# Performance work log

Measured on AMD Instinct MI355X. Metric: run time of the kernel, lower is better.

Reference implementation:

```python
import jax, jax.numpy as jnp
import numpy as np

B, C, H, W = 8, 384, 32, 32
NUM_HEADS = 8
HEAD_DIM = C // NUM_HEADS


def setup_inputs() -> dict:
    key = jax.random.key(0)
    k1, k2, k3, k4, k5 = jax.random.split(key, 5)
    s = 1.0 / np.sqrt(C)
    return {
        "x": jax.random.normal(k1, (B, C, H, W), dtype=jnp.float32),
        "w_qkv": jax.random.normal(k2, (3 * C, C), dtype=jnp.float32) * s,   # 1x1 conv == linear over channels
        "b_qkv": jax.random.normal(k3, (3 * C,), dtype=jnp.float32) * 0.01,
        "w_proj": jax.random.normal(k4, (C, C), dtype=jnp.float32) * s,
        "b_proj": jax.random.normal(k5, (C,), dtype=jnp.float32) * 0.01,
    }


def reference(x, w_qkv, b_qkv, w_proj, b_proj):
    b, c, h, w = x.shape
    n = h * w
    scale = HEAD_DIM ** (-0.5)
    # 1x1 conv qkv: (B, 3C, H, W)
    qkv = jnp.einsum('bchw,oc->bohw', x, w_qkv) + b_qkv[None, :, None, None]
    # 'b (three hd d) h0 w0 -> three b hd (h0 w0) d'
    qkv = qkv.reshape(b, 3, NUM_HEADS, HEAD_DIM, n)
    qkv = jnp.transpose(qkv, (1, 0, 2, 4, 3))  # (3, B, heads, N, d)
    q, k, v = qkv[0], qkv[1], qkv[2]
    attn = jnp.einsum('bhnd,bhmd->bhnm', q, k) * scale
    attn = jax.nn.softmax(attn, axis=-1)
    out = jnp.einsum('bhnm,bhmd->bhnd', attn, v)          # (B, heads, N, d)
    out = jnp.transpose(out, (0, 1, 3, 2)).reshape(b, c, h, w)  # b (hd d) h w
    out = jnp.einsum('bchw,oc->bohw', out, w_proj) + b_proj[None, :, None, None]
    return out
```

## Files before the change

### kernel.cpp

```cpp
#include <hip/hip_runtime.h>
#include <hip/hip_bf16.h>

typedef __hip_bfloat16 bf16;
typedef __bf16 bfx8 __attribute__((ext_vector_type(8)));
typedef float f32x4 __attribute__((ext_vector_type(4)));

#define Bk   8
#define Ck   384
#define NHk  8
#define Dk   48
#define Dp   64
#define Nk   1024
#define O3   1152


__device__ __forceinline__ void gload_lds16(const bf16* src, void* dst)
{
    __builtin_amdgcn_global_load_lds(
        (const __attribute__((address_space(1))) void*)src,
        (__attribute__((address_space(3))) void*)dst, 16, 0, 0);
}

__device__ __forceinline__ int pack2(float a, float b)
{
    bf16 ha = __float2bfloat16(a), hb = __float2bfloat16(b);
    unsigned lo = *(unsigned short*)&ha, hi = *(unsigned short*)&hb;
    return (int)(lo | (hi << 16));
}

__device__ __forceinline__ ushort4 pack4(float v0, float v1, float v2, float v3)
{
    bf16 h0 = __float2bfloat16(v0), h1 = __float2bfloat16(v1);
    bf16 h2 = __float2bfloat16(v2), h3 = __float2bfloat16(v3);
    ushort4 pk;
    pk.x = *(unsigned short*)&h0; pk.y = *(unsigned short*)&h1;
    pk.z = *(unsigned short*)&h2; pk.w = *(unsigned short*)&h3;
    return pk;
}

__global__ __launch_bounds__(256) void prep_kernel(
    const float* __restrict__ x, bf16* __restrict__ Xs,
    const float* __restrict__ wq, const float* __restrict__ wp,
    bf16* __restrict__ Wq, bf16* __restrict__ Wp,
    bf16* __restrict__ Qs, bf16* __restrict__ Ks)
{
    const int u = blockIdx.x * 256 + threadIdx.x;
    if (u < 393216) {
        int n = u & 1023, rest = u >> 10;
        int oct = rest % 48, b = rest / 48;
        const float* xb = x + (size_t)b * Ck * Nk;
        float f[8];
        #pragma unroll
        for (int e = 0; e < 8; ++e) f[e] = xb[(size_t)(oct * 8 + e) * Nk + n];
        int4 v = { pack2(f[0], f[1]), pack2(f[2], f[3]),
                   pack2(f[4], f[5]), pack2(f[6], f[7]) };
        bf16* dst = Xs + ((size_t)b * 64 + (n >> 4)) * 6144 + oct * 128 + (n & 15) * 8;
        *(int4*)dst = v;
    } else if (u < 448512) {
        int u1 = u - 393216;
        int o = u1 % 1152, oct = u1 / 1152;
        const float* src = wq + (size_t)o * Ck + oct * 8;
        int4 v = { pack2(src[0], src[1]), pack2(src[2], src[3]),
                   pack2(src[4], src[5]), pack2(src[6], src[7]) };
        bf16* dst = Wq + ((size_t)(o >> 4) * 48 + oct) * 128 + (o & 15) * 8;
        *(int4*)dst = v;
    } else if (u < 466944) {
        int u2 = u - 448512;
        int o = u2 % 384, oct = u2 / 384;
        const float* src = wp + (size_t)o * Ck + oct * 8;
        int4 v = { pack2(src[0], src[1]), pack2(src[2], src[3]),
                   pack2(src[4], src[5]), pack2(src[6], src[7]) };
        bf16* dst = Wp + ((size_t)(o >> 4) * 48 + oct) * 128 + (o & 15) * 8;
        *(int4*)dst = v;
    } else {
        int i = u - 466944;
        int buf = i >> 17;
        int r17 = i & 131071;
        int head = r17 >> 11;
        int r11 = r17 & 2047;
        int g = r11 >> 5, c5 = r11 & 31;
        int cd = 6 + (c5 >> 4), e = c5 & 15;
        bf16* p = (buf ? Ks : Qs) + (size_t)head * 65536 +
                  ((size_t)g * 8 + cd) * 128 + e * 8;
        *(int4*)p = (int4){0, 0, 0, 0};
    }
}

__global__ __launch_bounds__(256) void qkv_mfma_kernel(
    const bf16* __restrict__ Xs, const bf16* __restrict__ Wq,
    const float* __restrict__ bias,
    bf16* __restrict__ Qs, bf16* __restrict__ Ks, bf16* __restrict__ Vs)
{
    __shared__ __align__(16) bf16 Wl[24576];

    const int b    = blockIdx.z;
    const int by   = blockIdx.y;
    const int bx   = blockIdx.x;
    const int o0   = by * 64;
    const int n0   = bx * 128;
    const int wave = threadIdx.x >> 6;
    const int lane = threadIdx.x & 63;
    const int l15  = lane & 15, quad = lane >> 4;
    const int t3   = o0 / Ck;

    {
        const bf16* wsrc = Wq + (size_t)by * 24576;
        #pragma unroll
        for (int i = 0; i < 12; ++i) {
            int f = wave * 12 + i;
            gload_lds16(wsrc + f * 512 + lane * 8, (char*)Wl + f * 1024);
        }
    }

    const bf16* xg[2];
    #pragma unroll
    for (int i = 0; i < 2; ++i)
        xg[i] = Xs + ((size_t)(b * 64 + bx * 8 + wave * 2 + i) * 48) * 128 + lane * 8;
    const bf16* wl = Wl + lane * 8;

    f32x4 acc[8];
    #pragma unroll
    for (int i = 0; i < 8; ++i) acc[i] = (f32x4){0.f, 0.f, 0.f, 0.f};

    asm volatile("s_waitcnt vmcnt(0)" ::: "memory");
    __syncthreads();

    if (t3 < 2) {
        #pragma unroll
        for (int s = 0; s < 12; ++s) {
            bfx8 fx[2], fw[4];
            #pragma unroll
            for (int i = 0; i < 2; ++i) fx[i] = *(const bfx8*)(xg[i] + s * 512);
            #pragma unroll
            for (int j = 0; j < 4; ++j) fw[j] = *(const bfx8*)(wl + j * 6144 + s * 512);
            #pragma unroll
            for (int j = 0; j < 4; ++j)
                #pragma unroll
                for (int i = 0; i < 2; ++i)
                    acc[j * 2 + i] = __builtin_amdgcn_mfma_f32_16x16x32_bf16(
                        fw[j], fx[i], acc[j * 2 + i], 0, 0, 0);
        }
        const float qscale = 0.2082350964f;
        #pragma unroll
        for (int j = 0; j < 4; ++j) {
            int ob = o0 + j * 16 + quad * 4;
            float4 bi = *(const float4*)&bias[ob];
            int r  = ob - t3 * Ck;
            int hd = r / Dk, d0 = r - hd * Dk;
            bf16* hb = (t3 == 0 ? Qs : Ks) + (size_t)(b * NHk + hd) * 65536
                     + (d0 >> 3) * 128 + (d0 & 7);
            #pragma unroll
            for (int i = 0; i < 2; ++i) {
                int npos = n0 + wave * 32 + i * 16 + l15;
                f32x4 a = acc[j * 2 + i];
                float v0 = a[0] + bi.x, v1 = a[1] + bi.y;
                float v2 = a[2] + bi.z, v3 = a[3] + bi.w;
                if (t3 == 0) { v0 *= qscale; v1 *= qscale; v2 *= qscale; v3 *= qscale; }
                *(ushort4*)(hb + (size_t)(npos >> 4) * 1024 + (npos & 15) * 8) =
                    pack4(v0, v1, v2, v3);
            }
        }
    } else {
        #pragma unroll
        for (int s = 0; s < 12; ++s) {
            bfx8 fx[2], fw[4];
            #pragma unroll
            for (int i = 0; i < 2; ++i) fx[i] = *(const bfx8*)(xg[i] + s * 512);
            #pragma unroll
            for (int j = 0; j < 4; ++j) fw[j] = *(const bfx8*)(wl + j * 6144 + s * 512);
            #pragma unroll
            for (int i = 0; i < 2; ++i)
                #pragma unroll
                for (int j = 0; j < 4; ++j)
                    acc[i * 4 + j] = __builtin_amdgcn_mfma_f32_16x16x32_bf16(
                        fx[i], fw[j], acc[i * 4 + j], 0, 0, 0);
        }
        #pragma unroll
        for (int j = 0; j < 4; ++j) {
            int ov = o0 + j * 16 + l15;
            float bi = bias[ov];
            int r  = ov - 2 * Ck;
            int hd = r / Dk, d = r - hd * Dk;
            bf16* vbp = Vs + (size_t)(b * NHk + hd) * 49152
                      + (size_t)(d >> 4) * 16384 + (d & 15) * 8;
            #pragma unroll
            for (int i = 0; i < 2; ++i) {
                int npb = n0 + wave * 32 + i * 16 + quad * 4;
                f32x4 a = acc[i * 4 + j];
                *(ushort4*)(vbp + (size_t)(npb >> 3) * 128 + (npb & 7)) =
                    pack4(a[0] + bi, a[1] + bi, a[2] + bi, a[3] + bi);
            }
        }
    }
}

__global__ __launch_bounds__(256, 2) void attn_kernel(
    const bf16* __restrict__ Qs, const bf16* __restrict__ Ks,
    const bf16* __restrict__ Vs, bf16* __restrict__ AO)
{
    __shared__ __align__(16) bf16 KbL[2][4096];
    __shared__ __align__(16) bf16 VbL[2][3072];
    __shared__ __align__(16) short Ps[4 * 2 * 1152];
    __shared__ float sums[4][2][16];

    const int hd   = blockIdx.x;
    const int b    = blockIdx.y;
    const int bx   = blockIdx.z;
    const int t    = threadIdx.x;
    const int wave = t >> 6;
    const int lane = t & 63;
    const int l15  = lane & 15;
    const int quad = lane >> 4;
    const int grp16 = (bx * 4 + wave) * 2;

    const bf16* qb = Qs + (size_t)(b * NHk + hd) * 65536;
    const bf16* kb = Ks + (size_t)(b * NHk + hd) * 65536;
    const bf16* vb = Vs + (size_t)(b * NHk + hd) * 49152;

    auto stage = [&](int buf, int k0) {
        const bf16* ksrc = kb + (size_t)k0 * 64;
        const bf16* vsrc = vb + (size_t)(k0 >> 3) * 128;
        char* kdst = (char*)&KbL[buf][0];
        char* vdst = (char*)&VbL[buf][0];
        #pragma unroll
        for (int i = 0; i < 4; ++i) {
            const int l = wave + i * 4;
            if (l < 14) {
                const int piece = l >> 1, half = l & 1;
                const bf16* src; char* dst;
                if (piece < 4) {
                    src = ksrc + piece * 1024 + half * 512 + lane * 8;
                    dst = kdst + piece * 2048 + half * 1024;
                } else {
                    const int dc = piece - 4;
                    src = vsrc + (size_t)dc * 16384 + half * 512 + lane * 8;
                    dst = vdst + dc * 2048 + half * 1024;
                }
                gload_lds16(src, dst);
            }
        }
    };

    stage(0, 0);

    bfx8 bq[2][2];
    #pragma unroll
    for (int qt = 0; qt < 2; ++qt) {
        const bf16* qp = qb + ((size_t)(grp16 + qt) * 8 + quad) * 128 + l15 * 8;
        bq[qt][0] = *(const bfx8*)(qp);
        bq[qt][1] = *(const bfx8*)(qp + 512);
    }

    float l_run[2] = {0.f, 0.f};
    f32x4 oacc[2][3];
    #pragma unroll
    for (int qt = 0; qt < 2; ++qt)
        #pragma unroll
        for (int dc = 0; dc < 3; ++dc) oacc[qt][dc] = (f32x4){0.f, 0.f, 0.f, 0.f};

    short* const PsW[2] = { Ps + wave * 2304, Ps + wave * 2304 + 1152 };
    const int lo = quad * 128 + l15 * 8;

    asm volatile("s_waitcnt vmcnt(0)" ::: "memory");
    __syncthreads();

    auto step = [&](int buf, int k0, bool pf) {
        if (pf) stage(buf ^ 1, k0 + 64);

        const bf16* Kc = &KbL[buf][0];
        const bf16* Vc = &VbL[buf][0];

        f32x4 sf[2][4];
        #pragma unroll
        for (int s = 0; s < 4; ++s) {
            const bfx8 kf0 = *(const bfx8*)(Kc + s * 1024 + lo);
            const bfx8 kf1 = *(const bfx8*)(Kc + s * 1024 + 512 + lo);
            #pragma unroll
            for (int qt = 0; qt < 2; ++qt) {
                f32x4 z = (f32x4){0.f, 0.f, 0.f, 0.f};
                z = __builtin_amdgcn_mfma_f32_16x16x32_bf16(kf0, bq[qt][0], z, 0, 0, 0);
                z = __builtin_amdgcn_mfma_f32_16x16x32_bf16(kf1, bq[qt][1], z, 0, 0, 0);
                sf[qt][s] = z;
            }
        }

        #pragma unroll
        for (int qt = 0; qt < 2; ++qt) {
            float lsum = 0.f;
            #pragma unroll
            for (int s = 0; s < 4; ++s) {
                float e0 = __builtin_amdgcn_exp2f(sf[qt][s][0]);
                float e1 = __builtin_amdgcn_exp2f(sf[qt][s][1]);
                float e2 = __builtin_amdgcn_exp2f(sf[qt][s][2]);
                float e3 = __builtin_amdgcn_exp2f(sf[qt][s][3]);
                lsum += (e0 + e1) + (e2 + e3);
                *(ushort4*)&PsW[qt][l15 * 72 + s * 16 + quad * 4] =
                    pack4(e0, e1, e2, e3);
            }
            l_run[qt] += lsum;
        }

        #pragma unroll
        for (int qt = 0; qt < 2; ++qt) {
            const bfx8 ap0 = *(const bfx8*)&PsW[qt][l15 * 72 + quad * 8];
            const bfx8 ap1 = *(const bfx8*)&PsW[qt][l15 * 72 + 32 + quad * 8];
            #pragma unroll
            for (int dc = 0; dc < 3; ++dc) {
                const bfx8 bv0 = *(const bfx8*)(Vc + dc * 1024 + lo);
                const bfx8 bv1 = *(const bfx8*)(Vc + dc * 1024 + 512 + lo);
                oacc[qt][dc] = __builtin_amdgcn_mfma_f32_16x16x32_bf16(
                    ap0, bv0, oacc[qt][dc], 0, 0, 0);
                oacc[qt][dc] = __builtin_amdgcn_mfma_f32_16x16x32_bf16(
                    ap1, bv1, oacc[qt][dc], 0, 0, 0);
            }
        }

        asm volatile("s_waitcnt vmcnt(0)" ::: "memory");
        __syncthreads();
    };

    #pragma unroll 1
    for (int k0 = 0; k0 < Nk; k0 += 128) {
        step(0, k0, true);
        step(1, k0 + 64, k0 + 128 < Nk);
    }

    #pragma unroll
    for (int qt = 0; qt < 2; ++qt) {
        float lt = l_run[qt];
        lt += __shfl_xor(lt, 16, 64);
        lt += __shfl_xor(lt, 32, 64);
        sums[wave][qt][l15] = lt;
    }
    asm volatile("s_waitcnt lgkmcnt(0)" ::: "memory");

    #pragma unroll
    for (int qt = 0; qt < 2; ++qt) {
        short* OsW = PsW[qt];
        #pragma unroll
        for (int r = 0; r < 4; ++r) {
            int qi = quad * 4 + r;
            float rli = 1.0f / sums[wave][qt][qi];
            #pragma unroll
            for (int dcc = 0; dcc < 3; ++dcc) {
                bf16 hb = __float2bfloat16(oacc[qt][dcc][r] * rli);
                OsW[qi * 64 + dcc * 16 + l15] = *(short*)&hb;
            }
        }
    }
    asm volatile("s_waitcnt lgkmcnt(0)" ::: "memory");

    #pragma unroll
    for (int qt = 0; qt < 2; ++qt) {
        bf16* aob = AO + (((size_t)b * 64 + grp16 + qt) * 48 + hd * 6) * 128;
        short* OsW = PsW[qt];
        int u = lane;
        int4 v = *(const int4*)&OsW[(u & 15) * 64 + (u >> 4) * 8];
        *(int4*)(aob + u * 8) = v;
        if (lane < 32) {
            int u2 = 64 + lane;
            int4 v2 = *(const int4*)&OsW[(u2 & 15) * 64 + (u2 >> 4) * 8];
            *(int4*)(aob + u2 * 8) = v2;
        }
    }
}

__global__ __launch_bounds__(256) void proj_mfma_kernel(
    const bf16* __restrict__ AO, const bf16* __restrict__ Wp,
    const float* __restrict__ bias, float* __restrict__ out)
{
    __shared__ __align__(16) bf16 Wl[24576];

    const int b    = blockIdx.z;
    const int by   = blockIdx.y;
    const int bx   = blockIdx.x;
    const int o0   = by * 64;
    const int n0   = bx * 128;
    const int wave = threadIdx.x >> 6;
    const int lane = threadIdx.x & 63;
    const int l15  = lane & 15, quad = lane >> 4;

    {
        const bf16* wsrc = Wp + (size_t)by * 24576;
        #pragma unroll
        for (int i = 0; i < 12; ++i) {
            int f = wave * 12 + i;
            gload_lds16(wsrc + f * 512 + lane * 8, (char*)Wl + f * 1024);
        }
    }

    const bf16* ag[2];
    #pragma unroll
    for (int i = 0; i < 2; ++i)
        ag[i] = AO + ((size_t)(b * 64 + bx * 8 + wave * 2 + i) * 48) * 128 + lane * 8;
    const bf16* wl = Wl + lane * 8;

    f32x4 acc[8];
    #pragma unroll
    for (int i = 0; i < 8; ++i) acc[i] = (f32x4){0.f, 0.f, 0.f, 0.f};

    asm volatile("s_waitcnt vmcnt(0)" ::: "memory");
    __syncthreads();

    #pragma unroll
    for (int s = 0; s < 12; ++s) {
        bfx8 fx[2], fw[4];
        #pragma unroll
        for (int i = 0; i < 2; ++i) fx[i] = *(const bfx8*)(ag[i] + s * 512);
        #pragma unroll
        for (int j = 0; j < 4; ++j) fw[j] = *(const bfx8*)(wl + j * 6144 + s * 512);
        #pragma unroll
        for (int i = 0; i < 2; ++i)
            #pragma unroll
            for (int j = 0; j < 4; ++j)
                acc[i * 4 + j] = __builtin_amdgcn_mfma_f32_16x16x32_bf16(
                    fx[i], fw[j], acc[i * 4 + j], 0, 0, 0);
    }

    #pragma unroll
    for (int j = 0; j < 4; ++j) {
        int o = o0 + j * 16 + l15;
        float bi = bias[o];
        #pragma unroll
        for (int i = 0; i < 2; ++i) {
            int npb = n0 + wave * 32 + i * 16 + quad * 4;
            f32x4 a = acc[i * 4 + j];
            float4 v = { a[0] + bi, a[1] + bi, a[2] + bi, a[3] + bi };
            *(float4*)&out[((size_t)b * Ck + o) * Nk + npb] = v;
        }
    }
}

extern "C" void kernel_launch(void* const* d_in, const int* in_sizes, int n_in,
                              void* d_out, int out_size, void* d_ws, size_t ws_size,
                              hipStream_t stream)
{
    const float* x      = (const float*)d_in[0];
    const float* w_qkv  = (const float*)d_in[1];
    const float* b_qkv  = (const float*)d_in[2];
    const float* w_proj = (const float*)d_in[3];
    const float* b_proj = (const float*)d_in[4];
    float* out = (float*)d_out;

    const size_t XT_SEG = (size_t)Bk * Nk * Ck;
    const size_t WQ_SEG = (size_t)O3 * Ck;
    const size_t WP_SEG = (size_t)Ck * Ck;
    const size_t QK_SEG = (size_t)Bk * NHk * Nk * Dp;
    const size_t V_SEG  = (size_t)Bk * NHk * Dk * Nk;

    bf16* Xs = (bf16*)d_ws;
    bf16* Wq = Xs + XT_SEG;
    bf16* Wp = Wq + WQ_SEG;
    bf16* Qs = Wp + WP_SEG;
    bf16* Ks = Qs + QK_SEG;
    bf16* Vs = Ks + QK_SEG;
    bf16* AO = Vs + V_SEG;

    prep_kernel<<<2848, 256, 0, stream>>>(x, Xs, w_qkv, w_proj, Wq, Wp, Qs, Ks);
    qkv_mfma_kernel<<<dim3(Nk / 128, O3 / 64, Bk), 256, 0, stream>>>(
        Xs, Wq, b_qkv, Qs, Ks, Vs);
    attn_kernel<<<dim3(NHk, Bk, 8), 256, 0, stream>>>(Qs, Ks, Vs, AO);
    proj_mfma_kernel<<<dim3(Nk / 128, Ck / 64, Bk), 256, 0, stream>>>(
        AO, Wp, b_proj, out);
}
```

Baseline: 120.1 us.

## Triple-buffer attention K/V pipeline and enlarge GEMM tiles for qkv and proj

The attention kernel moves from double to triple buffering of K/V tiles in LDS. It waits with partial vmcnt counts and a single barrier per chunk, and raises wave priority around the MFMA sections, so loads stay in flight across iterations. The qkv and proj GEMM kernels now cover 256 positions per block instead of 128, with 16 accumulators per wave, a hoisted first X fragment load, and a reordered grid so batch is the fastest-varying dimension. This halves the number of GEMM blocks and the weight re-staging into LDS, but raises register pressure and leaves fewer blocks to fill the CUs.

```diff
diff --git a/kernel.cpp b/kernel.cpp
--- a/kernel.cpp
+++ b/kernel.cpp
@@ -86,18 +86,18 @@
     }
 }
 
-__global__ __launch_bounds__(256) void qkv_mfma_kernel(
+__global__ __launch_bounds__(256, 2) void qkv_mfma_kernel(
     const bf16* __restrict__ Xs, const bf16* __restrict__ Wq,
     const float* __restrict__ bias,
     bf16* __restrict__ Qs, bf16* __restrict__ Ks, bf16* __restrict__ Vs)
 {
     __shared__ __align__(16) bf16 Wl[24576];
 
-    const int b    = blockIdx.z;
+    const int b    = blockIdx.x;
     const int by   = blockIdx.y;
-    const int bx   = blockIdx.x;
+    const int bx   = blockIdx.z;
     const int o0   = by * 64;
-    const int n0   = bx * 128;
+    const int n0   = bx * 256;
     const int wave = threadIdx.x >> 6;
     const int lane = threadIdx.x & 63;
     const int l15  = lane & 15, quad = lane >> 4;
@@ -112,15 +112,19 @@
         }
     }
 
-    const bf16* xg[2];
-    #pragma unroll
-    for (int i = 0; i < 2; ++i)
-        xg[i] = Xs + ((size_t)(b * 64 + bx * 8 + wave * 2 + i) * 48) * 128 + lane * 8;
+    const bf16* xg[4];
+    #pragma unroll
+    for (int i = 0; i < 4; ++i)
+        xg[i] = Xs + ((size_t)(b * 64 + bx * 16 + wave * 4 + i) * 48) * 128 + lane * 8;
     const bf16* wl = Wl + lane * 8;
 
-    f32x4 acc[8];
-    #pragma unroll
-    for (int i = 0; i < 8; ++i) acc[i] = (f32x4){0.f, 0.f, 0.f, 0.f};
+    bfx8 fx0[4];
+    #pragma unroll
+    for (int i = 0; i < 4; ++i) fx0[i] = *(const bfx8*)(xg[i]);
+
+    f32x4 acc[16];
+    #pragma unroll
+    for (int i = 0; i < 16; ++i) acc[i] = (f32x4){0.f, 0.f, 0.f, 0.f};
 
     asm volatile("s_waitcnt vmcnt(0)" ::: "memory");
     __syncthreads();
@@ -128,17 +132,18 @@
     if (t3 < 2) {
         #pragma unroll
         for (int s = 0; s < 12; ++s) {
-            bfx8 fx[2], fw[4];
-            #pragma unroll
-            for (int i = 0; i < 2; ++i) fx[i] = *(const bfx8*)(xg[i] + s * 512);
+            bfx8 fx[4], fw[4];
+            #pragma unroll
+            for (int i = 0; i < 4; ++i)
+                fx[i] = (s == 0) ? fx0[i] : *(const bfx8*)(xg[i] + s * 512);
             #pragma unroll
             for (int j = 0; j < 4; ++j) fw[j] = *(const bfx8*)(wl + j * 6144 + s * 512);
             #pragma unroll
             for (int j = 0; j < 4; ++j)
                 #pragma unroll
-                for (int i = 0; i < 2; ++i)
-                    acc[j * 2 + i] = __builtin_amdgcn_mfma_f32_16x16x32_bf16(
-                        fw[j], fx[i], acc[j * 2 + i], 0, 0, 0);
+                for (int i = 0; i < 4; ++i)
+                    acc[j * 4 + i] = __builtin_amdgcn_mfma_f32_16x16x32_bf16(
+                        fw[j], fx[i], acc[j * 4 + i], 0, 0, 0);
         }
         const float qscale = 0.2082350964f;
         #pragma unroll
@@ -150,9 +155,9 @@
             bf16* hb = (t3 == 0 ? Qs : Ks) + (size_t)(b * NHk + hd) * 65536
                      + (d0 >> 3) * 128 + (d0 & 7);
             #pragma unroll
-            for (int i = 0; i < 2; ++i) {
-                int npos = n0 + wave * 32 + i * 16 + l15;
-                f32x4 a = acc[j * 2 + i];
+            for (int i = 0; i < 4; ++i) {
+                int npos = n0 + wave * 64 + i * 16 + l15;
+                f32x4 a = acc[j * 4 + i];
                 float v0 = a[0] + bi.x, v1 = a[1] + bi.y;
                 float v2 = a[2] + bi.z, v3 = a[3] + bi.w;
                 if (t3 == 0) { v0 *= qscale; v1 *= qscale; v2 *= qscale; v3 *= qscale; }
@@ -163,13 +168,14 @@
     } else {
         #pragma unroll
         for (int s = 0; s < 12; ++s) {
-            bfx8 fx[2], fw[4];
-            #pragma unroll
-            for (int i = 0; i < 2; ++i) fx[i] = *(const bfx8*)(xg[i] + s * 512);
+            bfx8 fx[4], fw[4];
+            #pragma unroll
+            for (int i = 0; i < 4; ++i)
+                fx[i] = (s == 0) ? fx0[i] : *(const bfx8*)(xg[i] + s * 512);
             #pragma unroll
             for (int j = 0; j < 4; ++j) fw[j] = *(const bfx8*)(wl + j * 6144 + s * 512);
             #pragma unroll
-            for (int i = 0; i < 2; ++i)
+            for (int i = 0; i < 4; ++i)
                 #pragma unroll
                 for (int j = 0; j < 4; ++j)
                     acc[i * 4 + j] = __builtin_amdgcn_mfma_f32_16x16x32_bf16(
@@ -184,8 +190,8 @@
             bf16* vbp = Vs + (size_t)(b * NHk + hd) * 49152
                       + (size_t)(d >> 4) * 16384 + (d & 15) * 8;
             #pragma unroll
-            for (int i = 0; i < 2; ++i) {
-                int npb = n0 + wave * 32 + i * 16 + quad * 4;
+            for (int i = 0; i < 4; ++i) {
+                int npb = n0 + wave * 64 + i * 16 + quad * 4;
                 f32x4 a = acc[i * 4 + j];
                 *(ushort4*)(vbp + (size_t)(npb >> 3) * 128 + (npb & 7)) =
                     pack4(a[0] + bi, a[1] + bi, a[2] + bi, a[3] + bi);
@@ -198,9 +204,9 @@
     const bf16* __restrict__ Qs, const bf16* __restrict__ Ks,
     const bf16* __restrict__ Vs, bf16* __restrict__ AO)
 {
-    __shared__ __align__(16) bf16 KbL[2][4096];
-    __shared__ __align__(16) bf16 VbL[2][3072];
-    __shared__ __align__(16) short Ps[4 * 2 * 1152];
+    __shared__ __align__(16) bf16 KbL[3][4096];
+    __shared__ __align__(16) bf16 VbL[3][3072];
+    __shared__ __align__(16) short Ps[4 * 2304];
     __shared__ float sums[4][2][16];
 
     const int hd   = blockIdx.x;
@@ -217,11 +223,11 @@
     const bf16* kb = Ks + (size_t)(b * NHk + hd) * 65536;
     const bf16* vb = Vs + (size_t)(b * NHk + hd) * 49152;
 
-    auto stage = [&](int buf, int k0) {
+    auto stage = [&](int slot, int k0) {
         const bf16* ksrc = kb + (size_t)k0 * 64;
         const bf16* vsrc = vb + (size_t)(k0 >> 3) * 128;
-        char* kdst = (char*)&KbL[buf][0];
-        char* vdst = (char*)&VbL[buf][0];
+        char* kdst = (char*)&KbL[slot][0];
+        char* vdst = (char*)&VbL[slot][0];
         #pragma unroll
         for (int i = 0; i < 4; ++i) {
             const int l = wave + i * 4;
@@ -242,6 +248,7 @@
     };
 
     stage(0, 0);
+    stage(1, 64);
 
     bfx8 bq[2][2];
     #pragma unroll
@@ -261,16 +268,24 @@
     short* const PsW[2] = { Ps + wave * 2304, Ps + wave * 2304 + 1152 };
     const int lo = quad * 128 + l15 * 8;
 
-    asm volatile("s_waitcnt vmcnt(0)" ::: "memory");
-    __syncthreads();
-
-    auto step = [&](int buf, int k0, bool pf) {
-        if (pf) stage(buf ^ 1, k0 + 64);
-
-        const bf16* Kc = &KbL[buf][0];
-        const bf16* Vc = &VbL[buf][0];
+    #pragma unroll 1
+    for (int c = 0; c < 16; ++c) {
+        if (c < 15) {
+            if (wave < 2) asm volatile("s_waitcnt vmcnt(4)" ::: "memory");
+            else          asm volatile("s_waitcnt vmcnt(3)" ::: "memory");
+        } else {
+            asm volatile("s_waitcnt vmcnt(0)" ::: "memory");
+        }
+        __builtin_amdgcn_sched_barrier(0);
+        __builtin_amdgcn_s_barrier();
+        __builtin_amdgcn_sched_barrier(0);
+
+        const int slot = c % 3;
+        const bf16* Kc = &KbL[slot][0];
+        const bf16* Vc = &VbL[slot][0];
 
         f32x4 sf[2][4];
+        __builtin_amdgcn_s_setprio(1);
         #pragma unroll
         for (int s = 0; s < 4; ++s) {
             const bfx8 kf0 = *(const bfx8*)(Kc + s * 1024 + lo);
@@ -283,6 +298,7 @@
                 sf[qt][s] = z;
             }
         }
+        __builtin_amdgcn_s_setprio(0);
 
         #pragma unroll
         for (int qt = 0; qt < 2; ++qt) {
@@ -300,6 +316,7 @@
             l_run[qt] += lsum;
         }
 
+        __builtin_amdgcn_s_setprio(1);
         #pragma unroll
         for (int qt = 0; qt < 2; ++qt) {
             const bfx8 ap0 = *(const bfx8*)&PsW[qt][l15 * 72 + quad * 8];
@@ -314,15 +331,9 @@
                     ap1, bv1, oacc[qt][dc], 0, 0, 0);
             }
         }
-
-        asm volatile("s_waitcnt vmcnt(0)" ::: "memory");
-        __syncthreads();
-    };
-
-    #pragma unroll 1
-    for (int k0 = 0; k0 < Nk; k0 += 128) {
-        step(0, k0, true);
-        step(1, k0 + 64, k0 + 128 < Nk);
+        __builtin_amdgcn_s_setprio(0);
+
+        if (c + 2 < 16) stage((c + 2) % 3, (c + 2) * 64);
     }
 
     #pragma unroll
@@ -365,17 +376,17 @@
     }
 }
 
-__global__ __launch_bounds__(256) void proj_mfma_kernel(
+__global__ __launch_bounds__(256, 2) void proj_mfma_kernel(
     const bf16* __restrict__ AO, const bf16* __restrict__ Wp,
     const float* __restrict__ bias, float* __restrict__ out)
 {
     __shared__ __align__(16) bf16 Wl[24576];
 
-    const int b    = blockIdx.z;
+    const int b    = blockIdx.x;
     const int by   = blockIdx.y;
-    const int bx   = blockIdx.x;
+    const int bx   = blockIdx.z;
     const int o0   = by * 64;
-    const int n0   = bx * 128;
+    const int n0   = bx * 256;
     const int wave = threadIdx.x >> 6;
     const int lane = threadIdx.x & 63;
     const int l15  = lane & 15, quad = lane >> 4;
@@ -389,28 +400,33 @@
         }
     }
 
-    const bf16* ag[2];
-    #pragma unroll
-    for (int i = 0; i < 2; ++i)
-        ag[i] = AO + ((size_t)(b * 64 + bx * 8 + wave * 2 + i) * 48) * 128 + lane * 8;
+    const bf16* ag[4];
+    #pragma unroll
+    for (int i = 0; i < 4; ++i)
+        ag[i] = AO + ((size_t)(b * 64 + bx * 16 + wave * 4 + i) * 48) * 128 + lane * 8;
     const bf16* wl = Wl + lane * 8;
 
-    f32x4 acc[8];
-    #pragma unroll
-    for (int i = 0; i < 8; ++i) acc[i] = (f32x4){0.f, 0.f, 0.f, 0.f};
+    bfx8 fx0[4];
+    #pragma unroll
+    for (int i = 0; i < 4; ++i) fx0[i] = *(const bfx8*)(ag[i]);
+
+    f32x4 acc[16];
+    #pragma unroll
+    for (int i = 0; i < 16; ++i) acc[i] = (f32x4){0.f, 0.f, 0.f, 0.f};
 
     asm volatile("s_waitcnt vmcnt(0)" ::: "memory");
     __syncthreads();
 
     #pragma unroll
     for (int s = 0; s < 12; ++s) {
-        bfx8 fx[2], fw[4];
-        #pragma unroll
-        for (int i = 0; i < 2; ++i) fx[i] = *(const bfx8*)(ag[i] + s * 512);
+        bfx8 fx[4], fw[4];
+        #pragma unroll
+        for (int i = 0; i < 4; ++i)
+            fx[i] = (s == 0) ? fx0[i] : *(const bfx8*)(ag[i] + s * 512);
         #pragma unroll
         for (int j = 0; j < 4; ++j) fw[j] = *(const bfx8*)(wl + j * 6144 + s * 512);
         #pragma unroll
-        for (int i = 0; i < 2; ++i)
+        for (int i = 0; i < 4; ++i)
             #pragma unroll
             for (int j = 0; j < 4; ++j)
                 acc[i * 4 + j] = __builtin_amdgcn_mfma_f32_16x16x32_bf16(
@@ -422,8 +438,8 @@
         int o = o0 + j * 16 + l15;
         float bi = bias[o];
         #pragma unroll
-        for (int i = 0; i < 2; ++i) {
-            int npb = n0 + wave * 32 + i * 16 + quad * 4;
+        for (int i = 0; i < 4; ++i) {
+            int npb = n0 + wave * 64 + i * 16 + quad * 4;
             f32x4 a = acc[i * 4 + j];
             float4 v = { a[0] + bi, a[1] + bi, a[2] + bi, a[3] + bi };
             *(float4*)&out[((size_t)b * Ck + o) * Nk + npb] = v;
@@ -457,9 +473,9 @@
     bf16* AO = Vs + V_SEG;
 
     prep_kernel<<<2848, 256, 0, stream>>>(x, Xs, w_qkv, w_proj, Wq, Wp, Qs, Ks);
-    qkv_mfma_kernel<<<dim3(Nk / 128, O3 / 64, Bk), 256, 0, stream>>>(
+    qkv_mfma_kernel<<<dim3(Bk, 18, 4), 256, 0, stream>>>(
         Xs, Wq, b_qkv, Qs, Ks, Vs);
     attn_kernel<<<dim3(NHk, Bk, 8), 256, 0, stream>>>(Qs, Ks, Vs, AO);
-    proj_mfma_kernel<<<dim3(Nk / 128, Ck / 64, Bk), 256, 0, stream>>>(
+    proj_mfma_kernel<<<dim3(Bk, 6, 4), 256, 0, stream>>>(
         AO, Wp, b_proj, out);
 }
```

Result: slower. 124.1 us (+3.3%).
